# Optimization experiments

Measured on AMD Instinct MI355X. Metric: run time of the kernel, lower is better.

The kernel has to match this reference:

```python
import jax, jax.numpy as jnp
import numpy as np

B, S, D, H = 2, 2048, 1024, 16
HD = D // H  # head dim = 64


def setup_inputs() -> dict:
    key = jax.random.key(0)
    ks = jax.random.split(key, 9)
    std = 0.02
    return {
        "hidden_states": jax.random.normal(ks[0], (B, S, D), jnp.float32),
        "wq": jax.random.normal(ks[1], (D, D), jnp.float32) * std,
        "bq": jnp.zeros((D,), jnp.float32),
        "wk": jax.random.normal(ks[2], (D, D), jnp.float32) * std,
        "bk": jnp.zeros((D,), jnp.float32),
        "wv": jax.random.normal(ks[3], (D, D), jnp.float32) * std,
        "bv": jnp.zeros((D,), jnp.float32),
        "wo": jax.random.normal(ks[4], (D, D), jnp.float32) * std,
        "bo": jnp.zeros((D,), jnp.float32),
    }


def reference(hidden_states, wq, bq, wk, bk, wv, bv, wo, bo):
    b, s, d = hidden_states.shape
    # projections (torch Linear: x @ W.T + b; here weights stored as [in,out]-equivalent transpose)
    q = hidden_states @ wq.T + bq
    k = hidden_states @ wk.T + bk
    v = hidden_states @ wv.T + bv
    # [b, h, s, hd]
    q = q.reshape(b, s, H, HD).transpose(0, 2, 1, 3)
    k = k.reshape(b, s, H, HD).transpose(0, 2, 1, 3)
    v = v.reshape(b, s, H, HD).transpose(0, 2, 1, 3)
    scores = jnp.einsum("bhqd,bhkd->bhqk", q, k) / jnp.sqrt(jnp.float32(HD))
    probs = jax.nn.softmax(scores, axis=-1)  # dropout p=0 (eval)
    ctx = jnp.einsum("bhqk,bhkd->bhqd", probs, v)
    ctx = ctx.transpose(0, 2, 1, 3).reshape(b, s, d)
    return ctx @ wo.T + bo
```

## Files before the change

kernel.cpp:

```cpp
#include <hip/hip_runtime.h>
#include <math.h>
#include <stdint.h>

constexpr int BB  = 2;
constexpr int SS  = 2048;
constexpr int DD  = 1024;
constexpr int HH  = 16;
constexpr int HDD = 64;
constexpr int MM  = BB * SS;

typedef uint16_t u16;
typedef __attribute__((ext_vector_type(4))) float    f32x4;
typedef __attribute__((ext_vector_type(8))) _Float16 f16x8;
typedef __attribute__((ext_vector_type(4))) _Float16 f16x4;
typedef __attribute__((ext_vector_type(2))) _Float16 f16x2;
typedef __attribute__((ext_vector_type(8))) short    s16x8;
typedef __attribute__((ext_vector_type(4))) unsigned int u32x4;

__device__ __forceinline__ u16 to_f16(float f) {
    const _Float16 h = (_Float16)f;
    return __builtin_bit_cast(u16, h);
}

__device__ __forceinline__ f32x4 mfma32(s16x8 a, s16x8 b, f32x4 c) {
    return __builtin_amdgcn_mfma_f32_16x16x32_f16(
        __builtin_bit_cast(f16x8, a), __builtin_bit_cast(f16x8, b), c, 0, 0, 0);
}
__device__ __forceinline__ f32x4 mfma32_ff(s16x8 a, f16x8 b, f32x4 c) {
    return __builtin_amdgcn_mfma_f32_16x16x32_f16(
        __builtin_bit_cast(f16x8, a), b, c, 0, 0, 0);
}

__device__ __forceinline__ void load_lds16(const void* g, void* l) {
    __builtin_amdgcn_global_load_lds(
        (const __attribute__((address_space(1))) void*)g,
        (__attribute__((address_space(3))) void*)l, 16, 0, 0);
}

__global__ __launch_bounds__(256) void cast_all(
    const float* __restrict__ x,
    const float* __restrict__ w0, const float* __restrict__ w1,
    const float* __restrict__ w2, const float* __restrict__ w3,
    u16* __restrict__ xb, u16* __restrict__ wb)
{
    const int blk = blockIdx.x, tid = threadIdx.x;
    const float* src; u16* dst; int idx;
    if (blk < 2048) { src = x; dst = xb; idx = blk * 256 + tid; }
    else {
        const int b2 = blk - 2048, which = b2 >> 9;
        src = (which == 0) ? w0 : (which == 1) ? w1 : (which == 2) ? w2 : w3;
        dst = wb + ((size_t)which << 20);
        idx = (b2 & 511) * 256 + tid;
    }
    const float4* in4 = (const float4*)src;
    const float4 a = in4[idx * 2], b = in4[idx * 2 + 1];
    s16x8 v;
    v[0] = (short)to_f16(a.x); v[1] = (short)to_f16(a.y);
    v[2] = (short)to_f16(a.z); v[3] = (short)to_f16(a.w);
    v[4] = (short)to_f16(b.x); v[5] = (short)to_f16(b.y);
    v[6] = (short)to_f16(b.z); v[7] = (short)to_f16(b.w);
    *(s16x8*)(dst + (size_t)idx * 8) = v;
}

template <bool SWAP>
__device__ __forceinline__ void kloop(
    const u16* __restrict__ Ag, const u16* __restrict__ Wg,
    u16* As, u16* Bs, const int K, const int c0, const int c1,
    const int lane, const int wm, const int wn, f32x4 (&acc)[4][4])
{
    load_lds16(Ag + (size_t)c0 * 16 * K, As + c0 * 512);
    load_lds16(Ag + (size_t)c1 * 16 * K, As + c1 * 512);
    load_lds16(Wg + (size_t)c0 * 16 * K, Bs + c0 * 512);
    load_lds16(Wg + (size_t)c1 * 16 * K, Bs + c1 * 512);

    for (int k0 = 0; k0 < K; k0 += 32) {
        const int buf = (k0 >> 5) & 1;
        __syncthreads();
        if (k0 + 32 < K) {
            const int nb_ = (buf ^ 1) * 4096;
            load_lds16(Ag + (size_t)c0 * 16 * K + k0 + 32, As + nb_ + c0 * 512);
            load_lds16(Ag + (size_t)c1 * 16 * K + k0 + 32, As + nb_ + c1 * 512);
            load_lds16(Wg + (size_t)c0 * 16 * K + k0 + 32, Bs + nb_ + c0 * 512);
            load_lds16(Wg + (size_t)c1 * 16 * K + k0 + 32, Bs + nb_ + c1 * 512);
        }
        const u16* Acur = As + buf * 4096;
        const u16* Bcur = Bs + buf * 4096;

        s16x8 af[4], bf4[4];
#pragma unroll
        for (int i = 0; i < 4; ++i) {
            const int row = wm + i * 16 + (lane & 15);
            const int u   = (lane >> 4) ^ (row & 3);
            af[i] = *(const s16x8*)(Acur + (size_t)row * 32 + u * 8);
        }
#pragma unroll
        for (int j = 0; j < 4; ++j) {
            const int row = wn + j * 16 + (lane & 15);
            const int u   = (lane >> 4) ^ (row & 3);
            bf4[j] = *(const s16x8*)(Bcur + (size_t)row * 32 + u * 8);
        }
#pragma unroll
        for (int i = 0; i < 4; ++i)
#pragma unroll
            for (int j = 0; j < 4; ++j)
                acc[i][j] = SWAP ? mfma32(bf4[j], af[i], acc[i][j])
                                 : mfma32(af[i], bf4[j], acc[i][j]);
    }
}

template <int MODE>
__global__ __launch_bounds__(256) void gemm_mfma(
    const u16* __restrict__ A, const u16* __restrict__ Wb,
    const float* __restrict__ b0, const float* __restrict__ b1,
    const float* __restrict__ b2,
    float* __restrict__ outf, u16* __restrict__ outq, u16* __restrict__ outv,
    const int K)
{
    __shared__ u16 As[2 * 128 * 32];
    __shared__ u16 Bs[2 * 128 * 32];

    const int tid = threadIdx.x, lane = tid & 63, wid = tid >> 6;
    const int quad = lane >> 4;
    const int bm = blockIdx.y * 128;
    const int nb = blockIdx.x * 128;
    const int which = nb >> 10;
    const int ncol  = nb & 1023;
    const u16* Wblk = Wb + ((size_t)which << 20) + (size_t)ncol * K;

    const int srow = lane >> 2;
    const int lu   = (lane & 3) ^ (srow & 3);
    const u16* Ag = A    + (size_t)(bm + srow) * K + lu * 8;
    const u16* Wg = Wblk + (size_t)srow       * K + lu * 8;
    const int c0 = wid * 2, c1 = c0 + 1;

    f32x4 acc[4][4];
#pragma unroll
    for (int i = 0; i < 4; ++i)
#pragma unroll
        for (int j = 0; j < 4; ++j) { f32x4 z = {0.f, 0.f, 0.f, 0.f}; acc[i][j] = z; }

    const int wm = (wid >> 1) * 64, wn = (wid & 1) * 64;
    const bool swap = (MODE == 0) || (which < 2);
    if (swap) kloop<true>(Ag, Wg, As, Bs, K, c0, c1, lane, wm, wn, acc);
    else      kloop<false>(Ag, Wg, As, Bs, K, c0, c1, lane, wm, wn, acc);

    if (MODE == 0) {
#pragma unroll
        for (int j = 0; j < 4; ++j) {
            const int n0 = nb + wn + 16 * j + quad * 4;
            const float4 bv = *(const float4*)&b0[n0];
#pragma unroll
            for (int i = 0; i < 4; ++i) {
                const int m = bm + wm + 16 * i + (lane & 15);
                f32x4 w = acc[i][j];
                w[0] += bv.x; w[1] += bv.y; w[2] += bv.z; w[3] += bv.w;
                *(f32x4*)&outf[(size_t)m * 1024 + n0] = w;
            }
        }
    } else if (which < 2) {
        const float* bias = which ? b1 : b0;
        const float scale = which ? 1.0f : 0.125f;
        u16* outb = outq + ((size_t)which << 22);
        const int h = (ncol + wn) >> 6;
#pragma unroll
        for (int j = 0; j < 4; ++j) {
            const int nl0 = ncol + wn + 16 * j + quad * 4;
            const float4 bv = *(const float4*)&bias[nl0];
            const int hd0 = 16 * j + quad * 4;
#pragma unroll
            for (int i = 0; i < 4; ++i) {
                const int m = bm + wm + 16 * i + (lane & 15);
                const int b_ = m >> 11, s = m & 2047;
                f16x4 w;
                w[0] = (_Float16)((acc[i][j][0] + bv.x) * scale);
                w[1] = (_Float16)((acc[i][j][1] + bv.y) * scale);
                w[2] = (_Float16)((acc[i][j][2] + bv.z) * scale);
                w[3] = (_Float16)((acc[i][j][3] + bv.w) * scale);
                *(f16x4*)&outb[(((size_t)(b_ * HH + h)) * SS + s) * HDD + hd0] = w;
            }
        }
    } else {
        const int kt = ((bm + wm) & 2047) >> 6;
        const int b_ = (bm + wm) >> 11;
#pragma unroll
        for (int j = 0; j < 4; ++j) {
            const int nl = ncol + wn + 16 * j + (lane & 15);
            const float bb = b2[nl];
            const int h = nl >> 6, hd = nl & 63;
            u16* vrow = outv + (((size_t)(b_ * HH + h)) * HDD + hd) * SS + kt * 64;
#pragma unroll
            for (int i = 0; i < 4; ++i) {
                const int p0 = (i >> 1) * 32 + quad * 8 + (i & 1) * 4;
                f16x4 w;
                w[0] = (_Float16)(acc[i][j][0] + bb);
                w[1] = (_Float16)(acc[i][j][1] + bb);
                w[2] = (_Float16)(acc[i][j][2] + bb);
                w[3] = (_Float16)(acc[i][j][3] + bb);
                *(f16x4*)&vrow[p0] = w;
            }
        }
    }
}

__global__ __launch_bounds__(512, 4) void attn_mfma(
    const u16* __restrict__ Q, const u16* __restrict__ Kg,
    const u16* __restrict__ Vt, u16* __restrict__ ctx)
{
    __shared__ u16 smem[32768];

    const int tid = threadIdx.x, lane = tid & 63, wid = tid >> 6;
    const int grp = wid >> 2, w4 = wid & 3;
    const int quad = lane >> 4;
    const int bh = blockIdx.y, q0 = blockIdx.x * 128;
    const u16* Qb = Q  + (size_t)bh * SS * HDD;
    const u16* Kb = Kg + (size_t)bh * SS * HDD + (size_t)grp * 1024 * HDD;
    const u16* Vb = Vt + (size_t)bh * HDD * SS + grp * 1024;

    u16* Kbase = smem + grp * 8192;
    u16* Vbase = smem + 16384 + grp * 8192;

    const int qa = q0 + w4 * 32 + (lane & 15);
    const s16x8 bq0a = *(const s16x8*)(Qb + (size_t)qa * HDD + quad * 8);
    const s16x8 bq1a = *(const s16x8*)(Qb + (size_t)qa * HDD + 32 + quad * 8);
    const s16x8 bq0b = *(const s16x8*)(Qb + (size_t)(qa + 16) * HDD + quad * 8);
    const s16x8 bq1b = *(const s16x8*)(Qb + (size_t)(qa + 16) * HDD + 32 + quad * 8);

    f32x4 oa[4], ob[4];
    f32x4 la4 = {0.f, 0.f, 0.f, 0.f}, lb4 = {0.f, 0.f, 0.f, 0.f};
#pragma unroll
    for (int m = 0; m < 4; ++m) {
        f32x4 z = {0.f, 0.f, 0.f, 0.f};
        oa[m] = z; ob[m] = z;
    }
    const s16x8 ones = {15360, 15360, 15360, 15360,
                        15360, 15360, 15360, 15360};

    const int c0 = w4 * 2, c1 = c0 + 1;
    const int r0 = (c0 * 64 + lane) >> 3, lu0 = ((lane & 7) ^ (r0 & 7));
    const int r1 = (c1 * 64 + lane) >> 3, lu1 = ((lane & 7) ^ (r1 & 7));
    const u16* Kp0 = Kb + (size_t)r0 * HDD + lu0 * 8;
    const u16* Kp1 = Kb + (size_t)r1 * HDD + lu1 * 8;
    const u16* Vp0 = Vb + (size_t)r0 * SS + lu0 * 8;
    const u16* Vp1 = Vb + (size_t)r1 * SS + lu1 * 8;

    load_lds16(Kp0, Kbase + c0 * 512);
    load_lds16(Kp1, Kbase + c1 * 512);
    load_lds16(Vp0, Vbase + c0 * 512);
    load_lds16(Vp1, Vbase + c1 * 512);

    for (int kt = 0; kt < 16; ++kt) {
        const int buf = kt & 1;
        __syncthreads();

        if (kt + 1 < 16) {
            const int nb_ = (buf ^ 1) * 4096;
            load_lds16(Kp0 + (size_t)(kt + 1) * 64 * HDD, Kbase + nb_ + c0 * 512);
            load_lds16(Kp1 + (size_t)(kt + 1) * 64 * HDD, Kbase + nb_ + c1 * 512);
            load_lds16(Vp0 + (kt + 1) * 64, Vbase + nb_ + c0 * 512);
            load_lds16(Vp1 + (kt + 1) * 64, Vbase + nb_ + c1 * 512);
        }
        const u16* Kbuf = Kbase + buf * 4096;
        const u16* Vbuf = Vbase + buf * 4096;

        f32x4 Sa[4], Sb[4];
#pragma unroll
        for (int j = 0; j < 4; ++j) {
            const int row = j * 16 + (lane & 15);
            const int sw = lane & 7;
            const s16x8 ak0 = *(const s16x8*)(Kbuf + (size_t)row * 64 + ((quad    ) ^ sw) * 8);
            const s16x8 ak1 = *(const s16x8*)(Kbuf + (size_t)row * 64 + ((quad + 4) ^ sw) * 8);
            f32x4 za = {0.f, 0.f, 0.f, 0.f};
            za = mfma32(ak0, bq0a, za);
            za = mfma32(ak1, bq1a, za);
            Sa[j] = za;
            f32x4 zb = {0.f, 0.f, 0.f, 0.f};
            zb = mfma32(ak0, bq0b, zb);
            zb = mfma32(ak1, bq1b, zb);
            Sb[j] = zb;
        }

        f16x8 pb0a, pb1a, pb0b, pb1b;
        {
            u32x4 u;
            u[0] = __builtin_bit_cast(unsigned int, __builtin_amdgcn_cvt_pkrtz(__expf(Sa[0][0]), __expf(Sa[0][1])));
            u[1] = __builtin_bit_cast(unsigned int, __builtin_amdgcn_cvt_pkrtz(__expf(Sa[0][2]), __expf(Sa[0][3])));
            u[2] = __builtin_bit_cast(unsigned int, __builtin_amdgcn_cvt_pkrtz(__expf(Sa[1][0]), __expf(Sa[1][1])));
            u[3] = __builtin_bit_cast(unsigned int, __builtin_amdgcn_cvt_pkrtz(__expf(Sa[1][2]), __expf(Sa[1][3])));
            pb0a = __builtin_bit_cast(f16x8, u);
            u[0] = __builtin_bit_cast(unsigned int, __builtin_amdgcn_cvt_pkrtz(__expf(Sa[2][0]), __expf(Sa[2][1])));
            u[1] = __builtin_bit_cast(unsigned int, __builtin_amdgcn_cvt_pkrtz(__expf(Sa[2][2]), __expf(Sa[2][3])));
            u[2] = __builtin_bit_cast(unsigned int, __builtin_amdgcn_cvt_pkrtz(__expf(Sa[3][0]), __expf(Sa[3][1])));
            u[3] = __builtin_bit_cast(unsigned int, __builtin_amdgcn_cvt_pkrtz(__expf(Sa[3][2]), __expf(Sa[3][3])));
            pb1a = __builtin_bit_cast(f16x8, u);
            u[0] = __builtin_bit_cast(unsigned int, __builtin_amdgcn_cvt_pkrtz(__expf(Sb[0][0]), __expf(Sb[0][1])));
            u[1] = __builtin_bit_cast(unsigned int, __builtin_amdgcn_cvt_pkrtz(__expf(Sb[0][2]), __expf(Sb[0][3])));
            u[2] = __builtin_bit_cast(unsigned int, __builtin_amdgcn_cvt_pkrtz(__expf(Sb[1][0]), __expf(Sb[1][1])));
            u[3] = __builtin_bit_cast(unsigned int, __builtin_amdgcn_cvt_pkrtz(__expf(Sb[1][2]), __expf(Sb[1][3])));
            pb0b = __builtin_bit_cast(f16x8, u);
            u[0] = __builtin_bit_cast(unsigned int, __builtin_amdgcn_cvt_pkrtz(__expf(Sb[2][0]), __expf(Sb[2][1])));
            u[1] = __builtin_bit_cast(unsigned int, __builtin_amdgcn_cvt_pkrtz(__expf(Sb[2][2]), __expf(Sb[2][3])));
            u[2] = __builtin_bit_cast(unsigned int, __builtin_amdgcn_cvt_pkrtz(__expf(Sb[3][0]), __expf(Sb[3][1])));
            u[3] = __builtin_bit_cast(unsigned int, __builtin_amdgcn_cvt_pkrtz(__expf(Sb[3][2]), __expf(Sb[3][3])));
            pb1b = __builtin_bit_cast(f16x8, u);
        }

        la4 = mfma32_ff(ones, pb0a, la4);
        la4 = mfma32_ff(ones, pb1a, la4);
        lb4 = mfma32_ff(ones, pb0b, lb4);
        lb4 = mfma32_ff(ones, pb1b, lb4);

#pragma unroll
        for (int m = 0; m < 4; ++m) {
            const int row = m * 16 + (lane & 15);
            const int sw = lane & 7;
            const s16x8 v0 = *(const s16x8*)(Vbuf + (size_t)row * 64 + ((quad    ) ^ sw) * 8);
            const s16x8 v1 = *(const s16x8*)(Vbuf + (size_t)row * 64 + ((quad + 4) ^ sw) * 8);
            oa[m] = mfma32_ff(v0, pb0a, oa[m]);
            oa[m] = mfma32_ff(v1, pb1a, oa[m]);
            ob[m] = mfma32_ff(v0, pb0b, ob[m]);
            ob[m] = mfma32_ff(v1, pb1b, ob[m]);
        }
    }

    __syncthreads();
    float* ep = (float*)smem;
    float* lp = ep + 8 * 1088;
    if (grp == 1) {
#pragma unroll
        for (int sub = 0; sub < 2; ++sub) {
            const float* src = (sub == 0) ? (const float*)&oa[0] : (const float*)&ob[0];
            float* base = ep + (w4 * 2 + sub) * 1088 + (lane & 15) * 68 + quad * 4;
#pragma unroll
            for (int m = 0; m < 4; ++m)
                *(f32x4*)(base + m * 16) = *(const f32x4*)(src + m * 4);
        }
        if (quad == 0) {
            lp[(w4 * 2 + 0) * 16 + (lane & 15)] = la4[0];
            lp[(w4 * 2 + 1) * 16 + (lane & 15)] = lb4[0];
        }
    }
    __syncthreads();
    if (grp == 0) {
        const int b_ = bh >> 4, h = bh & 15;
#pragma unroll
        for (int sub = 0; sub < 2; ++sub) {
            const f32x4* own = (sub == 0) ? &oa[0] : &ob[0];
            const float lown = (sub == 0) ? la4[0] : lb4[0];
            const float inv = 1.f / (lown + lp[(w4 * 2 + sub) * 16 + (lane & 15)]);
            const float* base = ep + (w4 * 2 + sub) * 1088 + (lane & 15) * 68 + quad * 4;
            const int s_idx = q0 + w4 * 32 + sub * 16 + (lane & 15);
            u16* orow = ctx + ((size_t)(b_ * SS + s_idx)) * DD + h * HDD;
#pragma unroll
            for (int m = 0; m < 4; ++m) {
                const f32x4 part = *(const f32x4*)(base + m * 16);
                f16x4 w;
#pragma unroll
                for (int r = 0; r < 4; ++r)
                    w[r] = (_Float16)((own[m][r] + part[r]) * inv);
                *(f16x4*)(orow + m * 16 + quad * 4) = w;
            }
        }
    }
}

extern "C" void kernel_launch(void* const* d_in, const int* in_sizes, int n_in,
                              void* d_out, int out_size, void* d_ws, size_t ws_size,
                              hipStream_t stream)
{
    const float* x  = (const float*)d_in[0];
    const float* wq = (const float*)d_in[1];
    const float* bq = (const float*)d_in[2];
    const float* wk = (const float*)d_in[3];
    const float* bk = (const float*)d_in[4];
    const float* wv = (const float*)d_in[5];
    const float* bv = (const float*)d_in[6];
    const float* wo = (const float*)d_in[7];
    const float* bo = (const float*)d_in[8];

    u16* xb   = (u16*)d_ws;
    u16* wb   = xb  + ((size_t)4  << 20);
    u16* qk   = wb  + ((size_t)4  << 20);
    u16* vtw  = qk  + ((size_t)8  << 20);
    u16* ctxb = vtw + ((size_t)4  << 20);

    cast_all<<<4096, 256, 0, stream>>>(x, wq, wk, wv, wo, xb, wb);

    gemm_mfma<1><<<dim3(24, 32), 256, 0, stream>>>(
        xb, wb, bq, bk, bv, nullptr, qk, vtw, DD);

    attn_mfma<<<dim3(16, 32), 512, 0, stream>>>(
        qk, qk + ((size_t)4 << 20), vtw, ctxb);

    gemm_mfma<0><<<dim3(8, 32), 256, 0, stream>>>(
        ctxb, wb + ((size_t)3 << 20), bo, nullptr, nullptr,
        (float*)d_out, nullptr, nullptr, DD);
}
```

Before: 208.5 us.

## Split GEMM K dimension across two wave groups with LDS reduction

The GEMM blocks grow to 512 threads, and two groups of four waves each handle half of the K range using separate LDS double buffers. At the end, group 1 writes its accumulators to shared memory and group 0 adds them before running the epilogue. The aim is more waves per output tile, to hide load latency in GEMMs with small grids (e.g. 256 blocks for the output projection). In exchange it adds a reduction through LDS, doubles LDS use to 64KB per block, and leaves half the threads idle during the epilogue.

```diff
diff --git a/kernel.cpp b/kernel.cpp
--- a/kernel.cpp
+++ b/kernel.cpp
@@ -13,7 +13,6 @@
 typedef __attribute__((ext_vector_type(4))) float    f32x4;
 typedef __attribute__((ext_vector_type(8))) _Float16 f16x8;
 typedef __attribute__((ext_vector_type(4))) _Float16 f16x4;
-typedef __attribute__((ext_vector_type(2))) _Float16 f16x2;
 typedef __attribute__((ext_vector_type(8))) short    s16x8;
 typedef __attribute__((ext_vector_type(4))) unsigned int u32x4;
 
@@ -65,26 +64,27 @@
 template <bool SWAP>
 __device__ __forceinline__ void kloop(
     const u16* __restrict__ Ag, const u16* __restrict__ Wg,
-    u16* As, u16* Bs, const int K, const int c0, const int c1,
+    u16* Abase, u16* Bbase, const int K, const int KH,
+    const int c0, const int c1,
     const int lane, const int wm, const int wn, f32x4 (&acc)[4][4])
 {
-    load_lds16(Ag + (size_t)c0 * 16 * K, As + c0 * 512);
-    load_lds16(Ag + (size_t)c1 * 16 * K, As + c1 * 512);
-    load_lds16(Wg + (size_t)c0 * 16 * K, Bs + c0 * 512);
-    load_lds16(Wg + (size_t)c1 * 16 * K, Bs + c1 * 512);
-
-    for (int k0 = 0; k0 < K; k0 += 32) {
+    load_lds16(Ag + (size_t)c0 * 16 * K, Abase + c0 * 512);
+    load_lds16(Ag + (size_t)c1 * 16 * K, Abase + c1 * 512);
+    load_lds16(Wg + (size_t)c0 * 16 * K, Bbase + c0 * 512);
+    load_lds16(Wg + (size_t)c1 * 16 * K, Bbase + c1 * 512);
+
+    for (int k0 = 0; k0 < KH; k0 += 32) {
         const int buf = (k0 >> 5) & 1;
         __syncthreads();
-        if (k0 + 32 < K) {
+        if (k0 + 32 < KH) {
             const int nb_ = (buf ^ 1) * 4096;
-            load_lds16(Ag + (size_t)c0 * 16 * K + k0 + 32, As + nb_ + c0 * 512);
-            load_lds16(Ag + (size_t)c1 * 16 * K + k0 + 32, As + nb_ + c1 * 512);
-            load_lds16(Wg + (size_t)c0 * 16 * K + k0 + 32, Bs + nb_ + c0 * 512);
-            load_lds16(Wg + (size_t)c1 * 16 * K + k0 + 32, Bs + nb_ + c1 * 512);
-        }
-        const u16* Acur = As + buf * 4096;
-        const u16* Bcur = Bs + buf * 4096;
+            load_lds16(Ag + (size_t)c0 * 16 * K + k0 + 32, Abase + nb_ + c0 * 512);
+            load_lds16(Ag + (size_t)c1 * 16 * K + k0 + 32, Abase + nb_ + c1 * 512);
+            load_lds16(Wg + (size_t)c0 * 16 * K + k0 + 32, Bbase + nb_ + c0 * 512);
+            load_lds16(Wg + (size_t)c1 * 16 * K + k0 + 32, Bbase + nb_ + c1 * 512);
+        }
+        const u16* Acur = Abase + buf * 4096;
+        const u16* Bcur = Bbase + buf * 4096;
 
         s16x8 af[4], bf4[4];
 #pragma unroll
@@ -109,29 +109,34 @@
 }
 
 template <int MODE>
-__global__ __launch_bounds__(256) void gemm_mfma(
+__global__ __launch_bounds__(512) void gemm_mfma(
     const u16* __restrict__ A, const u16* __restrict__ Wb,
     const float* __restrict__ b0, const float* __restrict__ b1,
     const float* __restrict__ b2,
     float* __restrict__ outf, u16* __restrict__ outq, u16* __restrict__ outv,
     const int K)
 {
-    __shared__ u16 As[2 * 128 * 32];
-    __shared__ u16 Bs[2 * 128 * 32];
+    __shared__ u16 smem[32768];
+    u16* As = smem;
+    u16* Bs = smem + 16384;
 
     const int tid = threadIdx.x, lane = tid & 63, wid = tid >> 6;
+    const int grp = wid >> 2, w4 = wid & 3;
     const int quad = lane >> 4;
     const int bm = blockIdx.y * 128;
     const int nb = blockIdx.x * 128;
     const int which = nb >> 10;
     const int ncol  = nb & 1023;
+    const int KH = K >> 1;
     const u16* Wblk = Wb + ((size_t)which << 20) + (size_t)ncol * K;
 
     const int srow = lane >> 2;
     const int lu   = (lane & 3) ^ (srow & 3);
-    const u16* Ag = A    + (size_t)(bm + srow) * K + lu * 8;
-    const u16* Wg = Wblk + (size_t)srow       * K + lu * 8;
-    const int c0 = wid * 2, c1 = c0 + 1;
+    const u16* Ag = A    + (size_t)(bm + srow) * K + grp * KH + lu * 8;
+    const u16* Wg = Wblk + (size_t)srow       * K + grp * KH + lu * 8;
+    const int c0 = w4 * 2, c1 = c0 + 1;
+    u16* Abase = As + grp * 8192;
+    u16* Bbase = Bs + grp * 8192;
 
     f32x4 acc[4][4];
 #pragma unroll
@@ -139,10 +144,28 @@
 #pragma unroll
         for (int j = 0; j < 4; ++j) { f32x4 z = {0.f, 0.f, 0.f, 0.f}; acc[i][j] = z; }
 
-    const int wm = (wid >> 1) * 64, wn = (wid & 1) * 64;
+    const int wm = (w4 >> 1) * 64, wn = (w4 & 1) * 64;
     const bool swap = (MODE == 0) || (which < 2);
-    if (swap) kloop<true>(Ag, Wg, As, Bs, K, c0, c1, lane, wm, wn, acc);
-    else      kloop<false>(Ag, Wg, As, Bs, K, c0, c1, lane, wm, wn, acc);
+    if (swap) kloop<true>(Ag, Wg, Abase, Bbase, K, KH, c0, c1, lane, wm, wn, acc);
+    else      kloop<false>(Ag, Wg, Abase, Bbase, K, KH, c0, c1, lane, wm, wn, acc);
+
+    __syncthreads();
+    float* rp = (float*)smem;
+    const int slot = (w4 * 64 + lane) * 4;
+    if (grp == 1) {
+#pragma unroll
+        for (int i = 0; i < 4; ++i)
+#pragma unroll
+            for (int j = 0; j < 4; ++j)
+                *(f32x4*)(rp + (i * 4 + j) * 1024 + slot) = acc[i][j];
+    }
+    __syncthreads();
+    if (grp != 0) return;
+#pragma unroll
+    for (int i = 0; i < 4; ++i)
+#pragma unroll
+        for (int j = 0; j < 4; ++j)
+            acc[i][j] += *(const f32x4*)(rp + (i * 4 + j) * 1024 + slot);
 
     if (MODE == 0) {
 #pragma unroll
@@ -385,13 +408,13 @@
 
     cast_all<<<4096, 256, 0, stream>>>(x, wq, wk, wv, wo, xb, wb);
 
-    gemm_mfma<1><<<dim3(24, 32), 256, 0, stream>>>(
+    gemm_mfma<1><<<dim3(24, 32), 512, 0, stream>>>(
         xb, wb, bq, bk, bv, nullptr, qk, vtw, DD);
 
     attn_mfma<<<dim3(16, 32), 512, 0, stream>>>(
         qk, qk + ((size_t)4 << 20), vtw, ctxb);
 
-    gemm_mfma<0><<<dim3(8, 32), 256, 0, stream>>>(
+    gemm_mfma<0><<<dim3(8, 32), 512, 0, stream>>>(
         ctxb, wb + ((size_t)3 << 20), bo, nullptr, nullptr,
         (float*)d_out, nullptr, nullptr, DD);
 }
```

Result: faster. 194.5 us (-6.7%).

## Deepen GEMM k-loop to a 4-stage LDS pipeline with explicit vmcnt waits

Applied to the files above, without the earlier changes.

Replaces the double-buffered GEMM k-loop with a 4-stage ring of LDS buffers, prefetching three tiles ahead. Each iteration waits with explicit s_waitcnt vmcnt thresholds and s_barrier, so only the oldest async loads must finish before compute starts. K is fixed at 1024 at compile time. This is meant to hide global-to-LDS latency in the projection GEMMs, at the cost of twice the LDS per block (64KB) and possibly lower occupancy. It also relies on the hand-written vmcnt counts matching the issued loads.

```diff
diff --git a/kernel.cpp b/kernel.cpp
--- a/kernel.cpp
+++ b/kernel.cpp
@@ -13,7 +13,6 @@
 typedef __attribute__((ext_vector_type(4))) float    f32x4;
 typedef __attribute__((ext_vector_type(8))) _Float16 f16x8;
 typedef __attribute__((ext_vector_type(4))) _Float16 f16x4;
-typedef __attribute__((ext_vector_type(2))) _Float16 f16x2;
 typedef __attribute__((ext_vector_type(8))) short    s16x8;
 typedef __attribute__((ext_vector_type(4))) unsigned int u32x4;
 
@@ -62,36 +61,43 @@
     *(s16x8*)(dst + (size_t)idx * 8) = v;
 }
 
+#define PIPE_BARRIER(N)                                               \
+    asm volatile("s_waitcnt vmcnt(" #N ") lgkmcnt(0)\n\ts_barrier" ::: "memory")
+
 template <bool SWAP>
-__device__ __forceinline__ void kloop(
+__device__ __forceinline__ void kloop_pipe(
     const u16* __restrict__ Ag, const u16* __restrict__ Wg,
-    u16* As, u16* Bs, const int K, const int c0, const int c1,
+    u16* As, u16* Bs, const int c0, const int c1,
     const int lane, const int wm, const int wn, f32x4 (&acc)[4][4])
 {
-    load_lds16(Ag + (size_t)c0 * 16 * K, As + c0 * 512);
-    load_lds16(Ag + (size_t)c1 * 16 * K, As + c1 * 512);
-    load_lds16(Wg + (size_t)c0 * 16 * K, Bs + c0 * 512);
-    load_lds16(Wg + (size_t)c1 * 16 * K, Bs + c1 * 512);
-
-    for (int k0 = 0; k0 < K; k0 += 32) {
-        const int buf = (k0 >> 5) & 1;
-        __syncthreads();
-        if (k0 + 32 < K) {
-            const int nb_ = (buf ^ 1) * 4096;
-            load_lds16(Ag + (size_t)c0 * 16 * K + k0 + 32, As + nb_ + c0 * 512);
-            load_lds16(Ag + (size_t)c1 * 16 * K + k0 + 32, As + nb_ + c1 * 512);
-            load_lds16(Wg + (size_t)c0 * 16 * K + k0 + 32, Bs + nb_ + c0 * 512);
-            load_lds16(Wg + (size_t)c1 * 16 * K + k0 + 32, Bs + nb_ + c1 * 512);
-        }
-        const u16* Acur = As + buf * 4096;
-        const u16* Bcur = Bs + buf * 4096;
+    constexpr int K = 1024, NITER = 32;
+#pragma unroll
+    for (int s = 0; s < 3; ++s) {
+        load_lds16(Ag + (size_t)c0 * 16 * K + s * 32, As + s * 4096 + c0 * 512);
+        load_lds16(Ag + (size_t)c1 * 16 * K + s * 32, As + s * 4096 + c1 * 512);
+        load_lds16(Wg + (size_t)c0 * 16 * K + s * 32, Bs + s * 4096 + c0 * 512);
+        load_lds16(Wg + (size_t)c1 * 16 * K + s * 32, Bs + s * 4096 + c1 * 512);
+    }
+    for (int i = 0; i < NITER; ++i) {
+        if (i < NITER - 2)       PIPE_BARRIER(8);
+        else if (i == NITER - 2) PIPE_BARRIER(4);
+        else                     PIPE_BARRIER(0);
+        if (i + 3 < NITER) {
+            const int st = (i + 3) & 3, k0 = (i + 3) * 32;
+            load_lds16(Ag + (size_t)c0 * 16 * K + k0, As + st * 4096 + c0 * 512);
+            load_lds16(Ag + (size_t)c1 * 16 * K + k0, As + st * 4096 + c1 * 512);
+            load_lds16(Wg + (size_t)c0 * 16 * K + k0, Bs + st * 4096 + c0 * 512);
+            load_lds16(Wg + (size_t)c1 * 16 * K + k0, Bs + st * 4096 + c1 * 512);
+        }
+        const u16* Acur = As + (i & 3) * 4096;
+        const u16* Bcur = Bs + (i & 3) * 4096;
 
         s16x8 af[4], bf4[4];
 #pragma unroll
-        for (int i = 0; i < 4; ++i) {
-            const int row = wm + i * 16 + (lane & 15);
+        for (int ii = 0; ii < 4; ++ii) {
+            const int row = wm + ii * 16 + (lane & 15);
             const int u   = (lane >> 4) ^ (row & 3);
-            af[i] = *(const s16x8*)(Acur + (size_t)row * 32 + u * 8);
+            af[ii] = *(const s16x8*)(Acur + (size_t)row * 32 + u * 8);
         }
 #pragma unroll
         for (int j = 0; j < 4; ++j) {
@@ -100,11 +106,11 @@
             bf4[j] = *(const s16x8*)(Bcur + (size_t)row * 32 + u * 8);
         }
 #pragma unroll
-        for (int i = 0; i < 4; ++i)
+        for (int ii = 0; ii < 4; ++ii)
 #pragma unroll
             for (int j = 0; j < 4; ++j)
-                acc[i][j] = SWAP ? mfma32(bf4[j], af[i], acc[i][j])
-                                 : mfma32(af[i], bf4[j], acc[i][j]);
+                acc[ii][j] = SWAP ? mfma32(bf4[j], af[ii], acc[ii][j])
+                                  : mfma32(af[ii], bf4[j], acc[ii][j]);
     }
 }
 
@@ -113,12 +119,12 @@
     const u16* __restrict__ A, const u16* __restrict__ Wb,
     const float* __restrict__ b0, const float* __restrict__ b1,
     const float* __restrict__ b2,
-    float* __restrict__ outf, u16* __restrict__ outq, u16* __restrict__ outv,
-    const int K)
+    float* __restrict__ outf, u16* __restrict__ outq, u16* __restrict__ outv)
 {
-    __shared__ u16 As[2 * 128 * 32];
-    __shared__ u16 Bs[2 * 128 * 32];
-
+    __shared__ u16 As[4 * 128 * 32];
+    __shared__ u16 Bs[4 * 128 * 32];
+
+    constexpr int K = 1024;
     const int tid = threadIdx.x, lane = tid & 63, wid = tid >> 6;
     const int quad = lane >> 4;
     const int bm = blockIdx.y * 128;
@@ -141,8 +147,8 @@
 
     const int wm = (wid >> 1) * 64, wn = (wid & 1) * 64;
     const bool swap = (MODE == 0) || (which < 2);
-    if (swap) kloop<true>(Ag, Wg, As, Bs, K, c0, c1, lane, wm, wn, acc);
-    else      kloop<false>(Ag, Wg, As, Bs, K, c0, c1, lane, wm, wn, acc);
+    if (swap) kloop_pipe<true>(Ag, Wg, As, Bs, c0, c1, lane, wm, wn, acc);
+    else      kloop_pipe<false>(Ag, Wg, As, Bs, c0, c1, lane, wm, wn, acc);
 
     if (MODE == 0) {
 #pragma unroll
@@ -166,7 +172,7 @@
         for (int j = 0; j < 4; ++j) {
             const int nl0 = ncol + wn + 16 * j + quad * 4;
             const float4 bv = *(const float4*)&bias[nl0];
-            const int hd0 = 16 * j + quad * 4;
+            const int hd0 = nl0 & 63;
 #pragma unroll
             for (int i = 0; i < 4; ++i) {
                 const int m = bm + wm + 16 * i + (lane & 15);
@@ -386,12 +392,12 @@
     cast_all<<<4096, 256, 0, stream>>>(x, wq, wk, wv, wo, xb, wb);
 
     gemm_mfma<1><<<dim3(24, 32), 256, 0, stream>>>(
-        xb, wb, bq, bk, bv, nullptr, qk, vtw, DD);
+        xb, wb, bq, bk, bv, nullptr, qk, vtw);
 
     attn_mfma<<<dim3(16, 32), 512, 0, stream>>>(
         qk, qk + ((size_t)4 << 20), vtw, ctxb);
 
     gemm_mfma<0><<<dim3(8, 32), 256, 0, stream>>>(
         ctxb, wb + ((size_t)3 << 20), bo, nullptr, nullptr,
-        (float*)d_out, nullptr, nullptr, DD);
-}
+        (float*)d_out, nullptr, nullptr);
+}
```

New measurement: 203.1 us. 1.03x faster.
